# Kernel tuning notes

Hardware: AMD Instinct MI355X
Metric: run time of the kernel (lower is better)

Reference implementation:

```python
import jax, jax.numpy as jnp
import numpy as np

B, T, E = 32, 512, 256
H = 512          # num_cells
REV_H = 10       # hardcoded LSTM(10)
CONV_C = 60      # hardcoded Conv1D(60)
FEAT = 3 * CONV_C + REV_H  # 190
D0 = 100
TEMP = 1e-5
EPS = 1e-20


def setup_inputs() -> dict:
    key = jax.random.key(0)
    ks = jax.random.split(key, 18)
    def g(k, shape, fan_in):
        return (jax.random.normal(k, shape, jnp.float32) / np.float32(np.sqrt(fan_in)))
    inp = {}
    inp["x"] = jax.random.normal(ks[0], (B, T, E), jnp.float32)
    # Conv1D kernels in WIO layout [k, in, out]
    inp["conv1_w"] = g(ks[1], (3, E, CONV_C), 3 * E)
    inp["conv1_b"] = jnp.zeros((CONV_C,), jnp.float32)
    inp["conv2_w"] = g(ks[2], (4, E, CONV_C), 4 * E)
    inp["conv2_b"] = jnp.zeros((CONV_C,), jnp.float32)
    inp["conv3_w"] = g(ks[3], (5, E, CONV_C), 5 * E)
    inp["conv3_b"] = jnp.zeros((CONV_C,), jnp.float32)
    # reverse LSTM(10)
    inp["rev_Wx"] = g(ks[4], (E, 4 * REV_H), E)
    inp["rev_Wh"] = g(ks[5], (REV_H, 4 * REV_H), REV_H)
    inp["rev_b"] = jnp.zeros((4 * REV_H,), jnp.float32)
    # gate MLP: Dense(100, relu) -> Dense(2)
    inp["d0_W"] = g(ks[6], (FEAT + E, D0), FEAT + E)
    inp["d0_b"] = jnp.zeros((D0,), jnp.float32)
    inp["d1_W"] = g(ks[7], (D0, 2), D0)
    inp["d1_b"] = jnp.zeros((2,), jnp.float32)
    # main LSTMCell(H)
    inp["cell_Wx"] = g(ks[8], (E, 4 * H), E)
    inp["cell_Wh"] = g(ks[9], (H, 4 * H), H)
    inp["cell_b"] = jnp.zeros((4 * H,), jnp.float32)
    # pre-sampled Gumbel(0,1) noise, one per (t, b, 2)
    U = jax.random.uniform(ks[10], (T, B, 2), jnp.float32, 1e-7, 1.0)
    inp["gumbel_noise"] = -jnp.log(-jnp.log(U + EPS) + EPS)
    return inp


def _lstm_scan(xseq, Wx, Wh, b):
    # xseq: [T, B, E] -> hs: [T, B, H]
    h_dim = Wh.shape[0]
    bsz = xseq.shape[1]
    def step(carry, xt):
        h, c = carry
        z = xt @ Wx + h @ Wh + b
        i, f, g_, o = jnp.split(z, 4, axis=-1)
        c = jax.nn.sigmoid(f) * c + jax.nn.sigmoid(i) * jnp.tanh(g_)
        h = jax.nn.sigmoid(o) * jnp.tanh(c)
        return (h, c), h
    init = (jnp.zeros((bsz, h_dim), xseq.dtype), jnp.zeros((bsz, h_dim), xseq.dtype))
    _, hs = jax.lax.scan(step, init, xseq)
    return hs


def reference(x, conv1_w, conv1_b, conv2_w, conv2_b, conv3_w, conv3_b,
              rev_Wx, rev_Wh, rev_b, d0_W, d0_b, d1_W, d1_b,
              cell_Wx, cell_Wh, cell_b, gumbel_noise):
    dn = ('NWC', 'WIO', 'NWC')
    def conv(w, b_):
        return jax.lax.conv_general_dilated(x, w, (1,), 'SAME', dimension_numbers=dn) + b_
    conved = jnp.concatenate([conv(conv1_w, conv1_b), conv(conv2_w, conv2_b), conv(conv3_w, conv3_b)], axis=-1)  # [B,T,180]
    # LSTM over reversed sequence (output NOT re-reversed, as in the original)
    x_rev = x[:, ::-1, :].transpose(1, 0, 2)               # [T,B,E]
    rev = _lstm_scan(x_rev, rev_Wx, rev_Wh, rev_b).transpose(1, 0, 2)  # [B,T,10]
    f_core = jnp.concatenate([conved, rev], axis=-1)        # [B,T,190]
    # f_all[:, t+1] for t in [0,T): shift left by one, pad a zero row at the end
    ff_seq = jnp.concatenate([f_core[:, 1:, :], jnp.zeros_like(f_core[:, :1, :])], axis=1)  # [B,T,190]

    bsz = x.shape[0]
    h_dim = cell_Wh.shape[0]
    xs = (x.transpose(1, 0, 2), ff_seq.transpose(1, 0, 2), gumbel_noise)

    def step(carry, inputs):
        h, c = carry
        xt, ff, gn = inputs
        # skip-gate logits -> Gumbel-softmax (temperature 1e-5)
        hid = jax.nn.relu(jnp.concatenate([ff, xt], axis=-1) @ d0_W + d0_b)
        pi = hid @ d1_W + d1_b                               # [B,2]
        d = jax.nn.softmax((pi + gn) / TEMP, axis=-1)        # [B,2]
        # LSTM cell candidate
        z = xt @ cell_Wx + h @ cell_Wh + cell_b
        i, f, g_, o = jnp.split(z, 4, axis=-1)
        c_cand = jax.nn.sigmoid(f) * c + jax.nn.sigmoid(i) * jnp.tanh(g_)
        h_cand = jax.nn.sigmoid(o) * jnp.tanh(c_cand)
        d0, d1 = d[:, :1], d[:, 1:]
        h_new = d0 * h_cand + d1 * h
        c_new = d0 * c_cand + d1 * c
        # output written each step is the (ungated) candidate h, per the source
        return (h_new, c_new), h_cand

    init = (jnp.zeros((bsz, h_dim), x.dtype), jnp.zeros((bsz, h_dim), x.dtype))
    _, outs = jax.lax.scan(step, init, xs)                  # [T,B,H]
    return outs.transpose(1, 0, 2)                          # [B,T,H]
```

## Files before the change

kernel.cpp:

```cpp
#include <hip/hip_runtime.h>
#include <math.h>

#define Bz 32
#define Tz 512
#define Ez 256
#define Hz 512
#define FCH 446

__device__ __forceinline__ float sigf(float x){ return 1.0f/(1.0f + __expf(-x)); }
__device__ __forceinline__ float tanhfast(float x){ return 1.0f - 2.0f/(__expf(2.0f*x) + 1.0f); }

__global__ __launch_bounds__(256) void k_conv(
    const float* __restrict__ x,
    const float* __restrict__ w1, const float* __restrict__ b1,
    const float* __restrict__ w2, const float* __restrict__ b2,
    const float* __restrict__ w3, const float* __restrict__ b3,
    const float* __restrict__ rwx,
    float* __restrict__ feat, float* __restrict__ rxw)
{
  __shared__ __align__(16) float xs[256*40];
  int b  = blockIdx.x >> 4;
  int t0 = (blockIdx.x & 15) * 32;
  int tid = threadIdx.x;
  for (int i = 0; i < 36; ++i){
    int t = t0 - 2 + i;
    xs[tid*40 + i] = (t >= 0 && t < Tz) ? x[(b*Tz + t)*Ez + tid] : 0.0f;
  }
  __syncthreads();
  for (int i = 0; i < 32; ++i){
    int t = t0 + i;
    feat[((size_t)t*Bz + b)*FCH + 190 + tid] = xs[tid*40 + i + 2];
  }
  int tq = tid & 7, cs = tid >> 3;
  float acc[6][4];
  float racc[2][4];
  #pragma unroll
  for (int ci = 0; ci < 6; ++ci){
    int c = cs + 32*ci;
    float bv = 0.0f;
    if (c < 60) bv = b1[c];
    else if (c < 120) bv = b2[c-60];
    else if (c < 180) bv = b3[c-120];
    acc[ci][0]=acc[ci][1]=acc[ci][2]=acc[ci][3]=bv;
  }
  #pragma unroll
  for (int ji = 0; ji < 2; ++ji){ racc[ji][0]=racc[ji][1]=racc[ji][2]=racc[ji][3]=0.0f; }

  for (int e = 0; e < 256; ++e){
    const float* xr = &xs[e*40 + 4*tq];
    float4 wa = *(const float4*)(xr);
    float4 wb = *(const float4*)(xr + 4);
    float wd[8] = {wa.x, wa.y, wa.z, wa.w, wb.x, wb.y, wb.z, wb.w};
    #pragma unroll
    for (int ci = 0; ci < 6; ++ci){
      int c = cs + 32*ci;
      if (c < 60){
        #pragma unroll
        for (int k = 0; k < 3; ++k){
          float wv = w1[(k*256 + e)*60 + c];
          #pragma unroll
          for (int j = 0; j < 4; ++j) acc[ci][j] = fmaf(wd[1 + j + k], wv, acc[ci][j]);
        }
      } else if (c < 120){
        int cc = c - 60;
        #pragma unroll
        for (int k = 0; k < 4; ++k){
          float wv = w2[(k*256 + e)*60 + cc];
          #pragma unroll
          for (int j = 0; j < 4; ++j) acc[ci][j] = fmaf(wd[1 + j + k], wv, acc[ci][j]);
        }
      } else if (c < 180){
        int cc = c - 120;
        #pragma unroll
        for (int k = 0; k < 5; ++k){
          float wv = w3[(k*256 + e)*60 + cc];
          #pragma unroll
          for (int j = 0; j < 4; ++j) acc[ci][j] = fmaf(wd[j + k], wv, acc[ci][j]);
        }
      }
    }
    #pragma unroll
    for (int ji = 0; ji < 2; ++ji){
      int jc = cs + 32*ji;
      if (jc < 40){
        float wv = rwx[e*40 + jc];
        #pragma unroll
        for (int j = 0; j < 4; ++j) racc[ji][j] = fmaf(wd[2 + j], wv, racc[ji][j]);
      }
    }
  }
  #pragma unroll
  for (int ci = 0; ci < 6; ++ci){
    int c = cs + 32*ci;
    if (c < 180){
      #pragma unroll
      for (int j = 0; j < 4; ++j){
        int t = t0 + 4*tq + j;
        if (t >= 1) feat[((size_t)(t-1)*Bz + b)*FCH + c] = acc[ci][j];
      }
    }
  }
  #pragma unroll
  for (int ji = 0; ji < 2; ++ji){
    int jc = cs + 32*ji;
    if (jc < 40){
      #pragma unroll
      for (int j = 0; j < 4; ++j){
        int t = t0 + 4*tq + j;
        rxw[((size_t)(511 - t)*Bz + b)*40 + jc] = racc[ji][j];
      }
    }
  }
}

__global__ __launch_bounds__(64) void k_rev(const float* __restrict__ rxw,
    const float* __restrict__ revWh, const float* __restrict__ revb, float* __restrict__ feat){
  int b = blockIdx.x;
  int j = threadIdx.x;
  float wreg[10];
  float bias = 0.0f;
  #pragma unroll
  for (int k = 0; k < 10; ++k) wreg[k] = 0.0f;
  if (j < 40){
    bias = revb[j];
    #pragma unroll
    for (int k = 0; k < 10; ++k) wreg[k] = revWh[k*40 + j];
  }
  float h[10];
  #pragma unroll
  for (int k = 0; k < 10; ++k) h[k] = 0.0f;
  float c = 0.0f;
  for (int s = 0; s < Tz; ++s){
    float z = bias + ((j < 40) ? rxw[(s*Bz + b)*40 + j] : 0.0f);
    #pragma unroll
    for (int k = 0; k < 10; ++k) z = fmaf(h[k], wreg[k], z);
    float a = (j >= 20 && j < 30) ? tanhfast(z) : sigf(z);
    float af = __shfl(a, j + 10);
    float ag = __shfl(a, j + 20);
    float ao = __shfl(a, j + 30);
    if (j < 10) c = af*c + a*ag;
    float hn = ao * tanhfast(c);
    #pragma unroll
    for (int k = 0; k < 10; ++k) h[k] = __shfl(hn, k);
    if (j < 10 && s >= 1) feat[((size_t)(s-1)*Bz + b)*FCH + 180 + j] = hn;
  }
}

__global__ __launch_bounds__(256) void k_hid(const float* __restrict__ feat,
    const float* __restrict__ d0W, const float* __restrict__ d0b, float* __restrict__ hid){
  __shared__ __align__(16) float fT[446*36];
  int r0 = blockIdx.x * 32;
  int tid = threadIdx.x;
  for (int r = 0; r < 32; ++r){
    fT[tid*36 + r] = feat[(size_t)(r0 + r)*FCH + tid];
    if (tid < 190) fT[(tid + 256)*36 + r] = feat[(size_t)(r0 + r)*FCH + tid + 256];
  }
  __syncthreads();
  int cs = tid & 31, rq = tid >> 5;
  if (cs < 25){
    float4 accv[4];
    #pragma unroll
    for (int jc = 0; jc < 4; ++jc) accv[jc] = make_float4(0.f,0.f,0.f,0.f);
    for (int k = 0; k < 446; ++k){
      float4 xv = *(const float4*)&fT[k*36 + 4*rq];
      float4 wv = *(const float4*)&d0W[k*100 + 4*cs];
      accv[0].x = fmaf(xv.x, wv.x, accv[0].x); accv[0].y = fmaf(xv.y, wv.x, accv[0].y);
      accv[0].z = fmaf(xv.z, wv.x, accv[0].z); accv[0].w = fmaf(xv.w, wv.x, accv[0].w);
      accv[1].x = fmaf(xv.x, wv.y, accv[1].x); accv[1].y = fmaf(xv.y, wv.y, accv[1].y);
      accv[1].z = fmaf(xv.z, wv.y, accv[1].z); accv[1].w = fmaf(xv.w, wv.y, accv[1].w);
      accv[2].x = fmaf(xv.x, wv.z, accv[2].x); accv[2].y = fmaf(xv.y, wv.z, accv[2].y);
      accv[2].z = fmaf(xv.z, wv.z, accv[2].z); accv[2].w = fmaf(xv.w, wv.z, accv[2].w);
      accv[3].x = fmaf(xv.x, wv.w, accv[3].x); accv[3].y = fmaf(xv.y, wv.w, accv[3].y);
      accv[3].z = fmaf(xv.z, wv.w, accv[3].z); accv[3].w = fmaf(xv.w, wv.w, accv[3].w);
    }
    #pragma unroll
    for (int i = 0; i < 4; ++i){
      int row = r0 + 4*rq + i;
      float4 o;
      float vi[4] = { i==0?accv[0].x:(i==1?accv[0].y:(i==2?accv[0].z:accv[0].w)),
                      i==0?accv[1].x:(i==1?accv[1].y:(i==2?accv[1].z:accv[1].w)),
                      i==0?accv[2].x:(i==1?accv[2].y:(i==2?accv[2].z:accv[2].w)),
                      i==0?accv[3].x:(i==1?accv[3].y:(i==2?accv[3].z:accv[3].w)) };
      o.x = fmaxf(vi[0] + d0b[4*cs+0], 0.0f);
      o.y = fmaxf(vi[1] + d0b[4*cs+1], 0.0f);
      o.z = fmaxf(vi[2] + d0b[4*cs+2], 0.0f);
      o.w = fmaxf(vi[3] + d0b[4*cs+3], 0.0f);
      *(float4*)&hid[(size_t)row*100 + 4*cs] = o;
    }
  }
}

__global__ __launch_bounds__(128) void k_pi(const float* __restrict__ hid,
    const float* __restrict__ d1W, const float* __restrict__ d1b,
    const float* __restrict__ gum, float* __restrict__ d0a, float* __restrict__ d1a){
  __shared__ float hidL[64*100];
  int r0 = blockIdx.x * 64;
  int tid = threadIdx.x;
  for (int i = 0; i < 50; ++i) hidL[tid + 128*i] = hid[(size_t)r0*100 + tid + 128*i];
  __syncthreads();
  int r = tid >> 1, pp = tid & 1;
  float s = d1b[pp];
  for (int m = 0; m < 100; ++m) s = fmaf(hidL[r*100 + m], d1W[m*2 + pp], s);
  int row = r0 + r;
  float a = (s + gum[row*2 + pp]) / 1e-5f;
  float other = __shfl_xor(a, 1);
  float mx = fmaxf(a, other);
  float ea = expf(a - mx), eb = expf(other - mx);
  float d = ea / (ea + eb);
  if (pp == 0) d0a[row] = d; else d1a[row] = d;
}

__global__ __launch_bounds__(256) void k_xz(const float* __restrict__ x,
    const float* __restrict__ Wx, const float* __restrict__ cb, float* __restrict__ xzG){
  __shared__ __align__(16) float xT[256*36];
  int t  = blockIdx.x & 511;
  int c0 = (blockIdx.x >> 9) * 128;
  int tid = threadIdx.x;
  for (int b = 0; b < 32; ++b){
    xT[tid*36 + b] = x[(b*Tz + t)*Ez + tid];
  }
  __syncthreads();
  int cs = tid & 31, rq = tid >> 5;
  float4 accv[4];
  #pragma unroll
  for (int jc = 0; jc < 4; ++jc) accv[jc] = make_float4(0.f,0.f,0.f,0.f);
  float4 wv = *(const float4*)&Wx[c0 + 4*cs];
  for (int e = 0; e < 256; ++e){
    float4 wc = wv;
    if (e != 255) wv = *(const float4*)&Wx[(e+1)*2048 + c0 + 4*cs];
    float4 xv = *(const float4*)&xT[e*36 + 4*rq];
    accv[0].x = fmaf(xv.x, wc.x, accv[0].x); accv[0].y = fmaf(xv.y, wc.x, accv[0].y);
    accv[0].z = fmaf(xv.z, wc.x, accv[0].z); accv[0].w = fmaf(xv.w, wc.x, accv[0].w);
    accv[1].x = fmaf(xv.x, wc.y, accv[1].x); accv[1].y = fmaf(xv.y, wc.y, accv[1].y);
    accv[1].z = fmaf(xv.z, wc.y, accv[1].z); accv[1].w = fmaf(xv.w, wc.y, accv[1].w);
    accv[2].x = fmaf(xv.x, wc.z, accv[2].x); accv[2].y = fmaf(xv.y, wc.z, accv[2].y);
    accv[2].z = fmaf(xv.z, wc.z, accv[2].z); accv[2].w = fmaf(xv.w, wc.z, accv[2].w);
    accv[3].x = fmaf(xv.x, wc.w, accv[3].x); accv[3].y = fmaf(xv.y, wc.w, accv[3].y);
    accv[3].z = fmaf(xv.z, wc.w, accv[3].z); accv[3].w = fmaf(xv.w, wc.w, accv[3].w);
  }
  #pragma unroll
  for (int jc = 0; jc < 4; ++jc){
    int col = c0 + 4*cs + jc;
    float bv = cb[col];
    float4 o = accv[jc];
    o.x += bv; o.y += bv; o.z += bv; o.w += bv;
    *(float4*)&xzG[(((size_t)rq*Tz + t)*2048 + col)*4] = o;
  }
}

__global__ __launch_bounds__(512, 2) void k_scan(
    const float* __restrict__ Wh, const float* __restrict__ xzG,
    const float* __restrict__ d0a, const float* __restrict__ d1a,
    float* __restrict__ hG,
    unsigned int* __restrict__ tags,
    float* __restrict__ out)
{
  __shared__ __align__(16) float hL[4*520];
  __shared__ __align__(16) float part[8*260];
  __shared__ float zL[256];
  __shared__ float hcandL[64];
  __shared__ float dv0L[2048];
  __shared__ float dv1L[2048];

  int tid = threadIdx.x;
  int g = blockIdx.x & 7;
  int m = blockIdx.x >> 3;
  int w = tid >> 6;
  int lane = tid & 63;

  float wreg[8][8];
  {
    int colbase = ((w >> 1) << 9) + (m << 4) + ((w & 1) << 3);
    #pragma unroll
    for (int j = 0; j < 8; ++j){
      const float4* wp = (const float4*)(Wh + (size_t)(lane*8 + j)*2048 + colbase);
      float4 a = wp[0], bq = wp[1];
      wreg[0][j]=a.x;  wreg[1][j]=a.y;  wreg[2][j]=a.z;  wreg[3][j]=a.w;
      wreg[4][j]=bq.x; wreg[5][j]=bq.y; wreg[6][j]=bq.z; wreg[7][j]=bq.w;
    }
  }
  for (int i = tid; i < 2048; i += 512){
    int tt = i >> 2, bb = i & 3;
    dv0L[i] = d0a[tt*32 + (g << 2) + bb];
    dv1L[i] = d1a[tt*32 + (g << 2) + bb];
  }

  int q0 = 2*lane;
  int sw = (q0 >> 3) & 3;
  int p0 = ((q0  ) ^ sw) << 2;
  int p1 = ((q0+1) ^ sw) << 2;

  int stb = tid >> 7, stq = tid & 127;
  int stp = (stq ^ ((stq >> 3) & 3)) << 2;
  const int hrow = 520;
  const unsigned int* mytag = tags + (g << 5) + (stq >> 2);

  int rcg = tid >> 2, rb = tid & 3;
  int rcol = ((rcg >> 4) << 9) + (m << 4) + (rcg & 15);
  size_t xzbase = ((size_t)g*Tz)*8192 + (size_t)rcol*4 + rb;

  float* hg0 = hG + (size_t)(g*2 + 0) * (4*512);
  float* hg1 = hG + (size_t)(g*2 + 1) * (4*512);

  float c_reg = 0.0f;

  for (int t = 0; t < Tz; ++t){
    const float* hcur = (t & 1) ? hg1 : hg0;
    float*       hnxt = (t & 1) ? hg0 : hg1;

    if (t == 0){
      *(float4*)&hL[stb*hrow + stp] = make_float4(0.f,0.f,0.f,0.f);
    } else {
      while (__hip_atomic_load(mytag, __ATOMIC_RELAXED, __HIP_MEMORY_SCOPE_AGENT)
             < (unsigned)t) { }
      const float* src = hcur + stb*512 + stq*4;
      float4 v;
      v.x = __hip_atomic_load(src+0, __ATOMIC_RELAXED, __HIP_MEMORY_SCOPE_AGENT);
      v.y = __hip_atomic_load(src+1, __ATOMIC_RELAXED, __HIP_MEMORY_SCOPE_AGENT);
      v.z = __hip_atomic_load(src+2, __ATOMIC_RELAXED, __HIP_MEMORY_SCOPE_AGENT);
      v.w = __hip_atomic_load(src+3, __ATOMIC_RELAXED, __HIP_MEMORY_SCOPE_AGENT);
      *(float4*)&hL[stb*hrow + stp] = v;
    }
    float xzv = 0.0f;
    if (tid < 256) xzv = xzG[xzbase + (size_t)t*8192];
    __syncthreads();

    float acc[8][4];
    #pragma unroll
    for (int ci = 0; ci < 8; ++ci)
      #pragma unroll
      for (int b = 0; b < 4; ++b) acc[ci][b] = 0.0f;
    #pragma unroll
    for (int b = 0; b < 4; ++b){
      const float* hr = &hL[b*hrow];
      float4 h0 = *(const float4*)(hr + p0);
      float4 h1 = *(const float4*)(hr + p1);
      float hv[8] = {h0.x,h0.y,h0.z,h0.w,h1.x,h1.y,h1.z,h1.w};
      #pragma unroll
      for (int j = 0; j < 8; ++j){
        #pragma unroll
        for (int ci = 0; ci < 8; ++ci)
          acc[ci][b] = fmaf(wreg[ci][j], hv[j], acc[ci][b]);
      }
    }

    float v16[16];
    {
      bool hi = (lane & 1);
      #pragma unroll
      for (int i = 0; i < 16; ++i){
        int ci = i >> 2, b = i & 3;
        float keep = hi ? acc[4+ci][b] : acc[ci][b];
        float send = hi ? acc[ci][b]   : acc[4+ci][b];
        v16[i] = keep + __shfl_xor(send, 1);
      }
    }
    float v8[8];
    {
      bool hi = (lane & 2);
      #pragma unroll
      for (int i = 0; i < 8; ++i){
        float keep = hi ? v16[8+i] : v16[i];
        float send = hi ? v16[i]   : v16[8+i];
        v8[i] = keep + __shfl_xor(send, 2);
      }
    }
    float v4[4];
    {
      bool hi = (lane & 4);
      #pragma unroll
      for (int b = 0; b < 4; ++b){
        float keep = hi ? v8[4+b] : v8[b];
        float send = hi ? v8[b]   : v8[4+b];
        v4[b] = keep + __shfl_xor(send, 4);
      }
    }
    {
      int e = ((lane & 1) << 2) | (lane & 2) | ((lane >> 2) & 1);
      float* pw = &part[(lane >> 3)*260 + ((8*w + e) << 2)];
      *(float4*)pw = make_float4(v4[0], v4[1], v4[2], v4[3]);
    }
    __syncthreads();

    if (tid < 256){
      float s0 = part[0*260 + tid] + part[1*260 + tid];
      float s1 = part[2*260 + tid] + part[3*260 + tid];
      float s2 = part[4*260 + tid] + part[5*260 + tid];
      float s3 = part[6*260 + tid] + part[7*260 + tid];
      zL[tid] = (s0+s1)+(s2+s3) + xzv;
    }
    __syncthreads();

    if (tid < 64){
      int jl = tid >> 2, bb = tid & 3;
      float zi = zL[      (jl << 2) + bb];
      float zf = zL[ 64 + (jl << 2) + bb];
      float zg = zL[128 + (jl << 2) + bb];
      float zo = zL[192 + (jl << 2) + bb];
      float dv0 = dv0L[(t << 2) + bb];
      float dv1 = dv1L[(t << 2) + bb];
      int hk = (m << 4) + jl;
      int hq = hk >> 2;
      int hph = (hq ^ ((hq >> 3) & 3)) << 2;
      float hold = hL[bb*hrow + hph + (hk & 3)];
      float ccand = sigf(zf)*c_reg + sigf(zi)*tanhfast(zg);
      float hcand = sigf(zo)*tanhfast(ccand);
      c_reg = dv0*ccand + dv1*c_reg;
      float hnew = dv0*hcand + dv1*hold;
      hcandL[(bb << 4) + jl] = hcand;
      __hip_atomic_store(hnxt + bb*512 + hk, hnew,
                         __ATOMIC_RELAXED, __HIP_MEMORY_SCOPE_AGENT);
    }
    __syncthreads();

    if (tid == 0){
      __hip_atomic_store(tags + (g << 5) + m, (unsigned)(t+1),
                         __ATOMIC_RELAXED, __HIP_MEMORY_SCOPE_AGENT);
    }
    if (tid >= 64 && tid < 80){
      int idx = tid - 64; int bb = idx >> 2, q = idx & 3;
      float4 v = *(const float4*)&hcandL[(bb << 4) + 4*q];
      *(float4*)(out + (size_t)((g << 2) + bb)*(Tz*Hz) + (size_t)t*Hz + (m << 4) + 4*q) = v;
    }
  }
}

extern "C" void kernel_launch(void* const* d_in, const int* in_sizes, int n_in,
                              void* d_out, int out_size, void* d_ws, size_t ws_size,
                              hipStream_t stream)
{
  const float* x       = (const float*)d_in[0];
  const float* conv1_w = (const float*)d_in[1];
  const float* conv1_b = (const float*)d_in[2];
  const float* conv2_w = (const float*)d_in[3];
  const float* conv2_b = (const float*)d_in[4];
  const float* conv3_w = (const float*)d_in[5];
  const float* conv3_b = (const float*)d_in[6];
  const float* rev_Wx  = (const float*)d_in[7];
  const float* rev_Wh  = (const float*)d_in[8];
  const float* rev_b   = (const float*)d_in[9];
  const float* d0_W    = (const float*)d_in[10];
  const float* d0_b    = (const float*)d_in[11];
  const float* d1_W    = (const float*)d_in[12];
  const float* d1_b    = (const float*)d_in[13];
  const float* cell_Wx = (const float*)d_in[14];
  const float* cell_Wh = (const float*)d_in[15];
  const float* cell_b  = (const float*)d_in[16];
  const float* gumbel  = (const float*)d_in[17];
  float* out = (float*)d_out;

  char* ws = (char*)d_ws;
  size_t off = 0;
  float* xzG  = (float*)(ws + off); off += (size_t)Tz*2048*Bz*4;
  float* feat = (float*)(ws + off); off += (size_t)Tz*Bz*FCH*4;
  float* rxw  = (float*)(ws + off); off += (size_t)Tz*Bz*40*4;
  float* hid  = (float*)(ws + off); off += (size_t)Tz*Bz*100*4;
  float* d0a  = (float*)(ws + off); off += (size_t)Tz*Bz*4;
  float* d1a  = (float*)(ws + off); off += (size_t)Tz*Bz*4;
  float* hG   = (float*)(ws + off); off += (size_t)8*2*4*512*4;
  unsigned int* tags = (unsigned int*)(ws + off); off += 8*32*4;

  hipMemsetAsync(feat + (size_t)(Tz-1)*Bz*FCH, 0, Bz*FCH*4, stream);
  hipMemsetAsync(tags, 0, 8*32*4, stream);

  k_conv<<<512, 256, 0, stream>>>(x, conv1_w, conv1_b, conv2_w, conv2_b,
                                  conv3_w, conv3_b, rev_Wx, feat, rxw);
  k_rev<<<32, 64, 0, stream>>>(rxw, rev_Wh, rev_b, feat);
  k_hid<<<512, 256, 0, stream>>>(feat, d0_W, d0_b, hid);
  k_pi<<<256, 128, 0, stream>>>(hid, d1_W, d1_b, gumbel, d0a, d1a);
  k_xz<<<8192, 256, 0, stream>>>(x, cell_Wx, cell_b, xzG);

  k_scan<<<256, 512, 0, stream>>>(cell_Wh, xzG, d0a, d1a, hG, tags, out);
}
```

Measured before the change: 2.896 ms.

## Fuse input projection into recurrent scan kernel with register-resident Wx

Removes the separate k_xz kernel and its large xzG intermediate buffer (T*B*4H floats) and computes x_t @ Wx inside the scan loop, using Wx slices held in registers and x rows double-buffered in shared memory. The x projection for step t is issued before the spin-wait on h, so it can overlap with the inter-block synchronisation latency. This trades extra per-step FMAs and higher register pressure (another 32 floats per thread at 2 blocks/CU) for eliminating a large global write and read pass and one kernel launch.

```diff
diff --git a/kernel.cpp b/kernel.cpp
--- a/kernel.cpp
+++ b/kernel.cpp
@@ -210,46 +210,9 @@
   if (pp == 0) d0a[row] = d; else d1a[row] = d;
 }
 
-__global__ __launch_bounds__(256) void k_xz(const float* __restrict__ x,
-    const float* __restrict__ Wx, const float* __restrict__ cb, float* __restrict__ xzG){
-  __shared__ __align__(16) float xT[256*36];
-  int t  = blockIdx.x & 511;
-  int c0 = (blockIdx.x >> 9) * 128;
-  int tid = threadIdx.x;
-  for (int b = 0; b < 32; ++b){
-    xT[tid*36 + b] = x[(b*Tz + t)*Ez + tid];
-  }
-  __syncthreads();
-  int cs = tid & 31, rq = tid >> 5;
-  float4 accv[4];
-  #pragma unroll
-  for (int jc = 0; jc < 4; ++jc) accv[jc] = make_float4(0.f,0.f,0.f,0.f);
-  float4 wv = *(const float4*)&Wx[c0 + 4*cs];
-  for (int e = 0; e < 256; ++e){
-    float4 wc = wv;
-    if (e != 255) wv = *(const float4*)&Wx[(e+1)*2048 + c0 + 4*cs];
-    float4 xv = *(const float4*)&xT[e*36 + 4*rq];
-    accv[0].x = fmaf(xv.x, wc.x, accv[0].x); accv[0].y = fmaf(xv.y, wc.x, accv[0].y);
-    accv[0].z = fmaf(xv.z, wc.x, accv[0].z); accv[0].w = fmaf(xv.w, wc.x, accv[0].w);
-    accv[1].x = fmaf(xv.x, wc.y, accv[1].x); accv[1].y = fmaf(xv.y, wc.y, accv[1].y);
-    accv[1].z = fmaf(xv.z, wc.y, accv[1].z); accv[1].w = fmaf(xv.w, wc.y, accv[1].w);
-    accv[2].x = fmaf(xv.x, wc.z, accv[2].x); accv[2].y = fmaf(xv.y, wc.z, accv[2].y);
-    accv[2].z = fmaf(xv.z, wc.z, accv[2].z); accv[2].w = fmaf(xv.w, wc.z, accv[2].w);
-    accv[3].x = fmaf(xv.x, wc.w, accv[3].x); accv[3].y = fmaf(xv.y, wc.w, accv[3].y);
-    accv[3].z = fmaf(xv.z, wc.w, accv[3].z); accv[3].w = fmaf(xv.w, wc.w, accv[3].w);
-  }
-  #pragma unroll
-  for (int jc = 0; jc < 4; ++jc){
-    int col = c0 + 4*cs + jc;
-    float bv = cb[col];
-    float4 o = accv[jc];
-    o.x += bv; o.y += bv; o.z += bv; o.w += bv;
-    *(float4*)&xzG[(((size_t)rq*Tz + t)*2048 + col)*4] = o;
-  }
-}
-
 __global__ __launch_bounds__(512, 2) void k_scan(
-    const float* __restrict__ Wh, const float* __restrict__ xzG,
+    const float* __restrict__ Wh, const float* __restrict__ Wx,
+    const float* __restrict__ cbias, const float* __restrict__ x,
     const float* __restrict__ d0a, const float* __restrict__ d1a,
     float* __restrict__ hG,
     unsigned int* __restrict__ tags,
@@ -261,6 +224,7 @@
   __shared__ float hcandL[64];
   __shared__ float dv0L[2048];
   __shared__ float dv1L[2048];
+  __shared__ __align__(16) float xL[2][4*256];
 
   int tid = threadIdx.x;
   int g = blockIdx.x & 7;
@@ -268,9 +232,10 @@
   int w = tid >> 6;
   int lane = tid & 63;
 
+  int colbase = ((w >> 1) << 9) + (m << 4) + ((w & 1) << 3);
+
   float wreg[8][8];
   {
-    int colbase = ((w >> 1) << 9) + (m << 4) + ((w & 1) << 3);
     #pragma unroll
     for (int j = 0; j < 8; ++j){
       const float4* wp = (const float4*)(Wh + (size_t)(lane*8 + j)*2048 + colbase);
@@ -279,11 +244,27 @@
       wreg[4][j]=bq.x; wreg[5][j]=bq.y; wreg[6][j]=bq.z; wreg[7][j]=bq.w;
     }
   }
+  float wxreg[8][4];
+  {
+    #pragma unroll
+    for (int j = 0; j < 4; ++j){
+      const float4* wp = (const float4*)(Wx + (size_t)(lane*4 + j)*2048 + colbase);
+      float4 a = wp[0], bq = wp[1];
+      wxreg[0][j]=a.x;  wxreg[1][j]=a.y;  wxreg[2][j]=a.z;  wxreg[3][j]=a.w;
+      wxreg[4][j]=bq.x; wxreg[5][j]=bq.y; wxreg[6][j]=bq.z; wxreg[7][j]=bq.w;
+    }
+  }
   for (int i = tid; i < 2048; i += 512){
     int tt = i >> 2, bb = i & 3;
     dv0L[i] = d0a[tt*32 + (g << 2) + bb];
     dv1L[i] = d1a[tt*32 + (g << 2) + bb];
   }
+  int xb = tid >> 6;
+  int xq = tid & 63;
+  size_t xrowbase = ((size_t)((g << 2) + (xb & 3)) * Tz) * Ez + 4*xq;
+  if (tid < 256){
+    *(float4*)&xL[0][xb*256 + 4*xq] = *(const float4*)&x[xrowbase];
+  }
 
   int q0 = 2*lane;
   int sw = (q0 >> 3) & 3;
@@ -295,18 +276,43 @@
   const int hrow = 520;
   const unsigned int* mytag = tags + (g << 5) + (stq >> 2);
 
-  int rcg = tid >> 2, rb = tid & 3;
+  int rcg = tid >> 2;
   int rcol = ((rcg >> 4) << 9) + (m << 4) + (rcg & 15);
-  size_t xzbase = ((size_t)g*Tz)*8192 + (size_t)rcol*4 + rb;
+  float cbv = (tid < 256) ? cbias[rcol] : 0.0f;
 
   float* hg0 = hG + (size_t)(g*2 + 0) * (4*512);
   float* hg1 = hG + (size_t)(g*2 + 1) * (4*512);
 
   float c_reg = 0.0f;
+
+  __syncthreads();
 
   for (int t = 0; t < Tz; ++t){
     const float* hcur = (t & 1) ? hg1 : hg0;
     float*       hnxt = (t & 1) ? hg0 : hg1;
+    const float* xlc  = xL[t & 1];
+
+    float acc[8][4];
+    #pragma unroll
+    for (int ci = 0; ci < 8; ++ci)
+      #pragma unroll
+      for (int b = 0; b < 4; ++b) acc[ci][b] = 0.0f;
+    #pragma unroll
+    for (int b = 0; b < 4; ++b){
+      float4 xv = *(const float4*)&xlc[b*256 + 4*lane];
+      float xd[4] = {xv.x, xv.y, xv.z, xv.w};
+      #pragma unroll
+      for (int j = 0; j < 4; ++j){
+        #pragma unroll
+        for (int ci = 0; ci < 8; ++ci)
+          acc[ci][b] = fmaf(wxreg[ci][j], xd[j], acc[ci][b]);
+      }
+    }
+
+    if (t < Tz-1 && tid < 256){
+      *(float4*)&xL[(t+1)&1][xb*256 + 4*xq] =
+          *(const float4*)&x[xrowbase + (size_t)(t+1)*Ez];
+    }
 
     if (t == 0){
       *(float4*)&hL[stb*hrow + stp] = make_float4(0.f,0.f,0.f,0.f);
@@ -321,15 +327,8 @@
       v.w = __hip_atomic_load(src+3, __ATOMIC_RELAXED, __HIP_MEMORY_SCOPE_AGENT);
       *(float4*)&hL[stb*hrow + stp] = v;
     }
-    float xzv = 0.0f;
-    if (tid < 256) xzv = xzG[xzbase + (size_t)t*8192];
     __syncthreads();
 
-    float acc[8][4];
-    #pragma unroll
-    for (int ci = 0; ci < 8; ++ci)
-      #pragma unroll
-      for (int b = 0; b < 4; ++b) acc[ci][b] = 0.0f;
     #pragma unroll
     for (int b = 0; b < 4; ++b){
       const float* hr = &hL[b*hrow];
@@ -387,7 +386,7 @@
       float s1 = part[2*260 + tid] + part[3*260 + tid];
       float s2 = part[4*260 + tid] + part[5*260 + tid];
       float s3 = part[6*260 + tid] + part[7*260 + tid];
-      zL[tid] = (s0+s1)+(s2+s3) + xzv;
+      zL[tid] = (s0+s1)+(s2+s3) + cbv;
     }
     __syncthreads();
 
@@ -451,7 +450,6 @@
 
   char* ws = (char*)d_ws;
   size_t off = 0;
-  float* xzG  = (float*)(ws + off); off += (size_t)Tz*2048*Bz*4;
   float* feat = (float*)(ws + off); off += (size_t)Tz*Bz*FCH*4;
   float* rxw  = (float*)(ws + off); off += (size_t)Tz*Bz*40*4;
   float* hid  = (float*)(ws + off); off += (size_t)Tz*Bz*100*4;
@@ -468,7 +466,6 @@
   k_rev<<<32, 64, 0, stream>>>(rxw, rev_Wh, rev_b, feat);
   k_hid<<<512, 256, 0, stream>>>(feat, d0_W, d0_b, hid);
   k_pi<<<256, 128, 0, stream>>>(hid, d1_W, d1_b, gumbel, d0a, d1a);
-  k_xz<<<8192, 256, 0, stream>>>(x, cell_Wx, cell_b, xzG);
-
-  k_scan<<<256, 512, 0, stream>>>(cell_Wh, xzG, d0a, d1a, hG, tags, out);
-}
+
+  k_scan<<<256, 512, 0, stream>>>(cell_Wh, cell_Wx, cell_b, x, d0a, d1a, hG, tags, out);
+}
```

Result: slower. 4.553 ms (+57.2%).

## Merge gate reduction into cell-update warp and drop two block barriers per step

Applied to the files above, without the earlier changes.

The recurrent scan kernel no longer reduces partial gate sums into a shared zL buffer in a separate phase. The first wavefront now sums the partials for all four gates directly and loads its own xz values early, while the previous h is kept in a register instead of being re-read from shared memory. The tag publish and output store now come from that same wavefront after an explicit s_waitcnt, removing two __syncthreads per timestep on the serial critical path. In exchange, 64 threads do more serial shared-memory reads, and ordering between h stores and the tag relies on the manual vmcnt wait within one wave.

```diff
diff --git a/kernel.cpp b/kernel.cpp
--- a/kernel.cpp
+++ b/kernel.cpp
@@ -257,8 +257,6 @@
 {
   __shared__ __align__(16) float hL[4*520];
   __shared__ __align__(16) float part[8*260];
-  __shared__ float zL[256];
-  __shared__ float hcandL[64];
   __shared__ float dv0L[2048];
   __shared__ float dv1L[2048];
 
@@ -295,18 +293,27 @@
   const int hrow = 520;
   const unsigned int* mytag = tags + (g << 5) + (stq >> 2);
 
-  int rcg = tid >> 2, rb = tid & 3;
-  int rcol = ((rcg >> 4) << 9) + (m << 4) + (rcg & 15);
-  size_t xzbase = ((size_t)g*Tz)*8192 + (size_t)rcol*4 + rb;
+  size_t xzb = (size_t)((m << 4) + (tid >> 2))*4 + (tid & 3);
 
   float* hg0 = hG + (size_t)(g*2 + 0) * (4*512);
   float* hg1 = hG + (size_t)(g*2 + 1) * (4*512);
 
   float c_reg = 0.0f;
+  float h_reg = 0.0f;
+
+  __syncthreads();
 
   for (int t = 0; t < Tz; ++t){
     const float* hcur = (t & 1) ? hg1 : hg0;
     float*       hnxt = (t & 1) ? hg0 : hg1;
+
+    float xz4[4] = {0.f, 0.f, 0.f, 0.f};
+    if (tid < 64){
+      size_t base = ((size_t)(g*Tz + t))*8192 + xzb;
+      #pragma unroll
+      for (int gi = 0; gi < 4; ++gi)
+        xz4[gi] = xzG[base + (size_t)gi*2048];
+    }
 
     if (t == 0){
       *(float4*)&hL[stb*hrow + stp] = make_float4(0.f,0.f,0.f,0.f);
@@ -321,8 +328,6 @@
       v.w = __hip_atomic_load(src+3, __ATOMIC_RELAXED, __HIP_MEMORY_SCOPE_AGENT);
       *(float4*)&hL[stb*hrow + stp] = v;
     }
-    float xzv = 0.0f;
-    if (tid < 256) xzv = xzG[xzbase + (size_t)t*8192];
     __syncthreads();
 
     float acc[8][4];
@@ -382,45 +387,34 @@
     }
     __syncthreads();
 
-    if (tid < 256){
-      float s0 = part[0*260 + tid] + part[1*260 + tid];
-      float s1 = part[2*260 + tid] + part[3*260 + tid];
-      float s2 = part[4*260 + tid] + part[5*260 + tid];
-      float s3 = part[6*260 + tid] + part[7*260 + tid];
-      zL[tid] = (s0+s1)+(s2+s3) + xzv;
-    }
-    __syncthreads();
-
     if (tid < 64){
       int jl = tid >> 2, bb = tid & 3;
-      float zi = zL[      (jl << 2) + bb];
-      float zf = zL[ 64 + (jl << 2) + bb];
-      float zg = zL[128 + (jl << 2) + bb];
-      float zo = zL[192 + (jl << 2) + bb];
+      float zv[4];
+      #pragma unroll
+      for (int gi = 0; gi < 4; ++gi){
+        int zi = ((gi << 4) | jl) << 2;
+        float s0 = part[0*260 + zi + bb] + part[1*260 + zi + bb];
+        float s1 = part[2*260 + zi + bb] + part[3*260 + zi + bb];
+        float s2 = part[4*260 + zi + bb] + part[5*260 + zi + bb];
+        float s3 = part[6*260 + zi + bb] + part[7*260 + zi + bb];
+        zv[gi] = (s0+s1)+(s2+s3) + xz4[gi];
+      }
       float dv0 = dv0L[(t << 2) + bb];
       float dv1 = dv1L[(t << 2) + bb];
+      float ccand = sigf(zv[1])*c_reg + sigf(zv[0])*tanhfast(zv[2]);
+      float hcand = sigf(zv[3])*tanhfast(ccand);
+      c_reg = dv0*ccand + dv1*c_reg;
+      float hnew = dv0*hcand + dv1*h_reg;
+      h_reg = hnew;
       int hk = (m << 4) + jl;
-      int hq = hk >> 2;
-      int hph = (hq ^ ((hq >> 3) & 3)) << 2;
-      float hold = hL[bb*hrow + hph + (hk & 3)];
-      float ccand = sigf(zf)*c_reg + sigf(zi)*tanhfast(zg);
-      float hcand = sigf(zo)*tanhfast(ccand);
-      c_reg = dv0*ccand + dv1*c_reg;
-      float hnew = dv0*hcand + dv1*hold;
-      hcandL[(bb << 4) + jl] = hcand;
       __hip_atomic_store(hnxt + bb*512 + hk, hnew,
                          __ATOMIC_RELAXED, __HIP_MEMORY_SCOPE_AGENT);
-    }
-    __syncthreads();
-
-    if (tid == 0){
-      __hip_atomic_store(tags + (g << 5) + m, (unsigned)(t+1),
-                         __ATOMIC_RELAXED, __HIP_MEMORY_SCOPE_AGENT);
-    }
-    if (tid >= 64 && tid < 80){
-      int idx = tid - 64; int bb = idx >> 2, q = idx & 3;
-      float4 v = *(const float4*)&hcandL[(bb << 4) + 4*q];
-      *(float4*)(out + (size_t)((g << 2) + bb)*(Tz*Hz) + (size_t)t*Hz + (m << 4) + 4*q) = v;
+      asm volatile("s_waitcnt vmcnt(0)" ::: "memory");
+      if (tid == 0){
+        __hip_atomic_store(tags + (g << 5) + m, (unsigned)(t+1),
+                           __ATOMIC_RELAXED, __HIP_MEMORY_SCOPE_AGENT);
+      }
+      out[(size_t)((g << 2) + bb)*(Tz*Hz) + (size_t)t*Hz + hk] = hcand;
     }
   }
 }
```

After: 3.888 ms. +34.3%, slower.
